# Kernel optimization log

Measured on AMD Instinct MI355X. Metric: run time of the kernel, lower is better.

## Reference

```python
import jax, jax.numpy as jnp
import numpy as np

C = 64
K = 3  # kernel_size
B, H, W = 8, 128, 128


def conv2d(x, w, b, pad, groups=1):
    y = jax.lax.conv_general_dilated(
        x, w, window_strides=(1, 1), padding=[(pad, pad), (pad, pad)],
        feature_group_count=groups, dimension_numbers=('NCHW', 'OIHW', 'NCHW'))
    return y + b[None, :, None, None]


def setup_inputs() -> dict:
    key = jax.random.key(0)
    ks = jax.random.split(key, 11)
    s3 = 1.0 / np.sqrt(C * 9)  # kaiming-ish scale for 3x3 convs
    inp = {
        'x':  jax.random.normal(ks[0], (B, C, H, W), jnp.float32),
        'w0': jax.random.normal(ks[1], (C, C, 3, 3), jnp.float32) * s3,
        'b0': jax.random.normal(ks[2], (C,), jnp.float32) * 0.01,
        'w1': jax.random.normal(ks[3], (C, 1, 3, 3), jnp.float32) * (1.0 / 3.0),  # depthwise
        'b1': jax.random.normal(ks[4], (C,), jnp.float32) * 0.01,
        'w2': jax.random.normal(ks[5], (1, 1, K), jnp.float32) * (1.0 / np.sqrt(K)),  # conv1d over channel axis
        'b2': jax.random.normal(ks[6], (1,), jnp.float32) * 0.01,
        'w3': jax.random.normal(ks[7], (C * K * K, C, 1, 1), jnp.float32) * (1.0 / np.sqrt(C)),  # 1x1 -> dynamic filters
        'b3': jax.random.normal(ks[8], (C * K * K,), jnp.float32) * 0.01,
        'wf': jax.random.normal(ks[9], (C, C, 3, 3), jnp.float32) * s3,
        'bf': jax.random.normal(ks[10], (C,), jnp.float32) * 0.01,
    }
    return inp


def reference(x, w0, b0, w1, b1, w2, b2, w3, b3, wf, bf):
    b, c, h, w = x.shape
    pre = x
    # conv0: dense 3x3
    x0 = conv2d(x, w0, b0, pad=1)
    # conv1: depthwise 3x3
    x1 = conv2d(x0, w1, b1, pad=1, groups=c)
    # ECA-style channel attention: global avg pool -> conv1d over channel dim
    m = jnp.mean(x0, axis=(2, 3))  # [b, c]
    x2 = jax.lax.conv_general_dilated(
        m[:, None, :], w2, window_strides=(1,), padding=[(K // 2, K // 2)],
        dimension_numbers=('NCH', 'OIH', 'NCH')) + b2[None, :, None]  # [b, 1, c]
    out = x1 + x2[:, 0, :, None, None]  # broadcast [b,c,1,1] over h,w
    # conv3: 1x1 producing per-pixel dynamic filters [b, c*9, h, w]
    fil = jnp.einsum('oc,bchw->bohw', w3[:, :, 0, 0], out) + b3[None, :, None, None]
    filter_x = fil.reshape(b, c, K * K, h, w)
    # unfold(x0): 3x3 patches, channel-major then row-major kernel positions
    xp = jnp.pad(x0, ((0, 0), (0, 0), (1, 1), (1, 1)))
    unfold_x = jnp.stack(
        [xp[:, :, i:i + h, j:j + w] for i in range(3) for j in range(3)], axis=2)  # [b,c,9,h,w]
    out = jnp.sum(unfold_x * filter_x, axis=2)  # per-pixel dynamic conv
    out = jnp.where(out >= 0, out, 0.2 * out)  # LeakyReLU(0.2)
    out = conv2d(out, wf, bf, pad=1) + pre
    return out
```

## Files before the change

### kernel.cpp

```cpp
#include <hip/hip_runtime.h>

#define BB 8
#define C 64
#define HH 128
#define WW 128
#define HW (HH*WW)

#define TS 72
#define NPX 324

typedef __attribute__((ext_vector_type(8))) short short8;
typedef __attribute__((ext_vector_type(4))) unsigned short us4;
typedef __attribute__((ext_vector_type(4))) float f32x4;

__device__ inline unsigned short f2bf(float f) {
    union { float f; unsigned u; } v; v.f = f;
    unsigned r = v.u + 0x7fff + ((v.u >> 16) & 1);
    return (unsigned short)(r >> 16);
}
__device__ inline float bf2f(unsigned short h) {
    union { unsigned u; float f; } v; v.u = ((unsigned)h) << 16;
    return v.f;
}

__global__ __launch_bounds__(256) void prep_kernel(
    const float* __restrict__ w0, const float* __restrict__ wf,
    const float* __restrict__ w3, const float* __restrict__ b3,
    unsigned short* __restrict__ wb0, unsigned short* __restrict__ wbf,
    unsigned short* __restrict__ wb3, float* __restrict__ b3r,
    float* __restrict__ m)
{
    const int t = blockIdx.x * 256 + threadIdx.x;
    for (int i = t; i < C*C*9; i += 128*256) {
        int p = i % 9; int rest = i / 9; int ci = rest % C; int oc = rest / C;
        wb0[(p*C + oc)*C + ci] = f2bf(w0[i]);
        wbf[(p*C + oc)*C + ci] = f2bf(wf[i]);
    }
    for (int i = t; i < 9*C*C; i += 128*256) {
        int j = i >> 12, oc = (i >> 6) & 63, k = i & 63;
        wb3[i] = f2bf(w3[(oc*9 + j)*C + k]);
    }
    for (int i = t; i < 9*C; i += 128*256) {
        int j = i >> 6, oc = i & 63;
        b3r[i] = b3[oc*9 + j];
    }
    for (int i = t; i < BB*C; i += 128*256) m[i] = 0.f;
}

template<bool FIRST>
__global__ __launch_bounds__(256) void conv_mfma_kernel(
    const void* __restrict__ in,
    const unsigned short* __restrict__ wb,
    const float* __restrict__ bias,
    const float* __restrict__ res,
    void* __restrict__ outp,
    float* __restrict__ m)
{
    __shared__ __align__(16) unsigned short tile[NPX*TS];
    __shared__ __align__(16) float sred[4][4][16];
    const int b  = blockIdx.z;
    const int h0 = blockIdx.y * 16;
    const int w0 = blockIdx.x * 16;
    const int t  = threadIdx.x;

    {
        const int pxi = t & 31, g = t >> 5;
        for (int px = pxi; px < NPX; px += 32) {
            int th = px / 18, tw = px - th*18;
            int gh = h0 + th - 1, gw = w0 + tw - 1;
            short8 v = {0,0,0,0,0,0,0,0};
            if ((unsigned)gh < HH && (unsigned)gw < WW) {
                if (FIRST) {
                    const float* sp = (const float*)in
                        + ((size_t)(b*C + g*8)*HW + gh*WW + gw);
#pragma unroll
                    for (int k = 0; k < 8; ++k) v[k] = (short)f2bf(sp[k*HW]);
                } else {
                    v = *(const short8*)((const unsigned short*)in
                        + ((size_t)(b*HW) + gh*WW + gw)*C + g*8);
                }
            }
            *(short8*)&tile[px*TS + g*8] = v;
        }
    }
    __syncthreads();

    const int wid = t >> 6, ln = t & 63;
    const int l15 = ln & 15, q = ln >> 4;

    f32x4 acc[4][4];
#pragma unroll
    for (int mg = 0; mg < 4; ++mg)
#pragma unroll
        for (int nt = 0; nt < 4; ++nt) acc[mg][nt] = (f32x4){0.f,0.f,0.f,0.f};

#pragma unroll
    for (int p = 0; p < 9; ++p) {
        const int dh = p / 3, dw = p % 3;
#pragma unroll
        for (int ks = 0; ks < 2; ++ks) {
            short8 bfrag[4];
#pragma unroll
            for (int nt = 0; nt < 4; ++nt)
                bfrag[nt] = *(const short8*)&wb[((size_t)(p*C) + nt*16 + l15)*C + ks*32 + q*8];
            short8 afrag[4];
#pragma unroll
            for (int mg = 0; mg < 4; ++mg) {
                const int r = wid*4 + mg;
                afrag[mg] = *(const short8*)&tile[((r+dh)*18 + l15 + dw)*TS + ks*32 + q*8];
            }
#pragma unroll
            for (int mg = 0; mg < 4; ++mg)
#pragma unroll
                for (int nt = 0; nt < 4; ++nt) {
                    if (FIRST)
                        acc[mg][nt] = __builtin_amdgcn_mfma_f32_16x16x32_bf16(
                            afrag[mg], bfrag[nt], acc[mg][nt], 0, 0, 0);
                    else
                        acc[mg][nt] = __builtin_amdgcn_mfma_f32_16x16x32_bf16(
                            bfrag[nt], afrag[mg], acc[mg][nt], 0, 0, 0);
                }
        }
    }

    if (FIRST) {
        unsigned short* x0o = (unsigned short*)outp;
#pragma unroll
        for (int nt = 0; nt < 4; ++nt) {
            const int oc = nt*16 + l15;
            const float bv = bias[oc];
            float s = 0.f;
#pragma unroll
            for (int mg = 0; mg < 4; ++mg) {
                const int hh = h0 + wid*4 + mg;
#pragma unroll
                for (int reg = 0; reg < 4; ++reg) {
                    const int wwp = w0 + q*4 + reg;
                    const unsigned short sv = f2bf(acc[mg][nt][reg] + bv);
                    x0o[((size_t)(b*HW) + hh*WW + wwp)*C + oc] = sv;
                    s += bf2f(sv);
                }
            }
            s += __shfl_xor(s, 16);
            s += __shfl_xor(s, 32);
            if (q == 0) sred[wid][nt][l15] = s;
        }
        __syncthreads();
        if (t < 64) {
            float s = sred[0][t >> 4][t & 15] + sred[1][t >> 4][t & 15]
                    + sred[2][t >> 4][t & 15] + sred[3][t >> 4][t & 15];
            atomicAdd(&m[b*C + t], s * (1.f/(float)HW));
        }
    } else {
        float* outg = (float*)outp;
#pragma unroll
        for (int mg = 0; mg < 4; ++mg) {
            const int hh = h0 + wid*4 + mg;
#pragma unroll
            for (int nt = 0; nt < 4; ++nt) {
                const f32x4 bv4 = *(const f32x4*)&bias[nt*16 + q*4];
#pragma unroll
                for (int reg = 0; reg < 4; ++reg) {
                    const int oc = nt*16 + q*4 + reg;
                    const size_t base = (size_t)(b*C + oc)*HW + hh*WW + w0 + l15;
                    outg[base] = acc[mg][nt][reg] + bv4[reg] + res[base];
                }
            }
        }
    }
}

__global__ __launch_bounds__(256) void fused_kernel(
    const unsigned short* __restrict__ x0,
    const float* __restrict__ w1, const float* __restrict__ b1,
    const float* __restrict__ w2, const float* __restrict__ b2,
    const unsigned short* __restrict__ wb3,
    const float* __restrict__ b3r,
    const float* __restrict__ m,
    unsigned short* __restrict__ y)
{
    __shared__ __align__(16) unsigned short tile[NPX*TS];
    __shared__ __align__(16) unsigned short alds[256*64];
    __shared__ __align__(16) float att[64];
    const int b  = blockIdx.z;
    const int h0 = blockIdx.y * 16;
    const int w0 = blockIdx.x * 16;
    const int t  = threadIdx.x;

    if (t < 64) {
        const float mc = m[b*C + t];
        const float mp = (t > 0)  ? m[b*C + t - 1] : 0.f;
        const float mn = (t < 63) ? m[b*C + t + 1] : 0.f;
        att[t] = b1[t] + fmaf(w2[0], mp, fmaf(w2[1], mc, fmaf(w2[2], mn, b2[0])));
    }
    {
        const int pxi = t & 31, g = t >> 5;
        for (int px = pxi; px < NPX; px += 32) {
            int th = px / 18, tw = px - th*18;
            int gh = h0 + th - 1, gw = w0 + tw - 1;
            short8 v = {0,0,0,0,0,0,0,0};
            if ((unsigned)gh < HH && (unsigned)gw < WW)
                v = *(const short8*)&x0[((size_t)(b*HW) + gh*WW + gw)*C + g*8];
            *(short8*)&tile[px*TS + g*8] = v;
        }
    }
    __syncthreads();

    const int r = t >> 4, cc = t & 15;
    const unsigned short* tbase = tile + (r*18 + cc)*TS;

    float outv[64];
#pragma unroll
    for (int g = 0; g < 8; ++g) {
        float dw8[8];
#pragma unroll
        for (int k = 0; k < 8; ++k) dw8[k] = 0.f;
#pragma unroll
        for (int j = 0; j < 9; ++j) {
            short8 v = *(const short8*)&tbase[((j/3)*18 + (j%3))*TS + g*8];
#pragma unroll
            for (int k = 0; k < 8; ++k)
                dw8[k] = fmaf(w1[(g*8+k)*9 + j], bf2f((unsigned short)v[k]), dw8[k]);
        }
#pragma unroll
        for (int k = 0; k < 8; ++k) {
            const int c = g*8 + k;
            outv[c] = dw8[k] + att[c];
        }
    }

    {
        const int sw = t & 7;
#pragma unroll
        for (int g = 0; g < 8; ++g) {
            short8 v;
#pragma unroll
            for (int k = 0; k < 8; ++k) v[k] = (short)f2bf(outv[g*8 + k]);
            *(short8*)&alds[t*64 + ((g ^ sw) * 8)] = v;
        }
    }
    __syncthreads();

    const int wid = t >> 6, ln = t & 63;
    const int l15 = ln & 15, q = ln >> 4;

    short8 afrag[4][2];
#pragma unroll
    for (int mg = 0; mg < 4; ++mg) {
        const int px = (wid*4 + mg)*16 + l15;
        const int sw = px & 7;
#pragma unroll
        for (int ks = 0; ks < 2; ++ks)
            afrag[mg][ks] = *(const short8*)&alds[px*64 + (((ks*4 + q) ^ sw) * 8)];
    }

    f32x4 y_acc[4][4];
#pragma unroll
    for (int mg = 0; mg < 4; ++mg)
#pragma unroll
        for (int nt = 0; nt < 4; ++nt) y_acc[mg][nt] = (f32x4){0.f,0.f,0.f,0.f};

#pragma unroll 1
    for (int j = 0; j < 9; ++j) {
        const int dh = j / 3, dw = j - dh*3;
#pragma unroll
        for (int ntoc = 0; ntoc < 4; ++ntoc) {
            const short8 bf0 = *(const short8*)&wb3[((size_t)(j*64 + ntoc*16 + l15))*64 + q*8];
            const short8 bf1 = *(const short8*)&wb3[((size_t)(j*64 + ntoc*16 + l15))*64 + 32 + q*8];
            const f32x4 b3v4 = *(const f32x4*)&b3r[j*64 + ntoc*16 + q*4];
#pragma unroll
            for (int mg = 0; mg < 4; ++mg) {
                f32x4 a = b3v4;
                a = __builtin_amdgcn_mfma_f32_16x16x32_bf16(bf0, afrag[mg][0], a, 0, 0, 0);
                a = __builtin_amdgcn_mfma_f32_16x16x32_bf16(bf1, afrag[mg][1], a, 0, 0, 0);
                const int rr = wid*4 + mg;
                const us4 pv = *(const us4*)
                    &tile[((rr+dh)*18 + l15 + dw)*TS + ntoc*16 + q*4];
#pragma unroll
                for (int reg = 0; reg < 4; ++reg)
                    y_acc[mg][ntoc][reg] = fmaf(a[reg], bf2f(pv[reg]), y_acc[mg][ntoc][reg]);
            }
        }
    }

    __syncthreads();
    unsigned short* ybuf = alds;
#pragma unroll
    for (int mg = 0; mg < 4; ++mg) {
        const int rr = wid*4 + mg;
        const int px = rr*16 + l15;
        const int swy = (px & 7) << 1;
#pragma unroll
        for (int ntoc = 0; ntoc < 4; ++ntoc) {
            us4 ov;
#pragma unroll
            for (int reg = 0; reg < 4; ++reg) {
                float v = y_acc[mg][ntoc][reg];
                v = (v >= 0.f) ? v : 0.2f * v;
                ov[reg] = f2bf(v);
            }
            const int slot = (ntoc*4 + q) ^ swy;
            *(us4*)&ybuf[px*64 + slot*4] = ov;
        }
    }
    __syncthreads();
    for (int id = t; id < 2048; id += 256) {
        int px = id >> 3, g = id & 7;
        const int swy = (px & 7) << 1;
        short8 v = *(const short8*)&ybuf[px*64 + ((2*g) ^ swy)*4];
        int rr = px >> 4, cw = px & 15;
        *(short8*)&y[((size_t)(b*HW) + (h0+rr)*WW + (w0+cw))*C + g*8] = v;
    }
}

extern "C" void kernel_launch(void* const* d_in, const int* in_sizes, int n_in,
                              void* d_out, int out_size, void* d_ws, size_t ws_size,
                              hipStream_t stream) {
    const float* x  = (const float*)d_in[0];
    const float* w0 = (const float*)d_in[1];
    const float* b0 = (const float*)d_in[2];
    const float* w1 = (const float*)d_in[3];
    const float* b1 = (const float*)d_in[4];
    const float* w2 = (const float*)d_in[5];
    const float* b2 = (const float*)d_in[6];
    const float* w3 = (const float*)d_in[7];
    const float* b3 = (const float*)d_in[8];
    const float* wf = (const float*)d_in[9];
    const float* bf = (const float*)d_in[10];
    float* out = (float*)d_out;

    unsigned short* x0  = (unsigned short*)d_ws;
    unsigned short* y   = x0 + (size_t)BB*HW*C;
    float*          m   = (float*)(y + (size_t)BB*HW*C);
    unsigned short* wb0 = (unsigned short*)(m + BB*C);
    unsigned short* wbf = wb0 + 9*C*C;
    unsigned short* wb3 = wbf + 9*C*C;
    float*          b3r = (float*)(wb3 + 9*C*C);

    prep_kernel<<<128, 256, 0, stream>>>(w0, wf, w3, b3, wb0, wbf, wb3, b3r, m);
    conv_mfma_kernel<true><<<dim3(8,8,8), 256, 0, stream>>>(x, wb0, b0, nullptr, x0, m);
    fused_kernel<<<dim3(8,8,8), 256, 0, stream>>>(x0, w1, b1, w2, b2, wb3, b3r, m, y);
    conv_mfma_kernel<false><<<dim3(8,8,8), 256, 0, stream>>>(y, wbf, bf, x, out, nullptr);
}
```

Measured before the change: 214.0 us.

## Halve spatial tile height and split output channels across wave pairs

Shrinks each block's tile from 16x16 to 8x16 pixels and doubles the grid. Waves now split work 2x2 by row group and output-channel half, and the depthwise stage splits channels across two thread halves. This cuts per-block LDS and accumulator registers, and the grid grows to 1024 blocks, which should raise occupancy and CU coverage on a 256-CU part. In exchange the halo is a larger share of each tile, adding redundant loads, and each wave reloads A fragments for fewer output channels.

```diff
diff --git a/kernel.cpp b/kernel.cpp
--- a/kernel.cpp
+++ b/kernel.cpp
@@ -7,7 +7,7 @@
 #define HW (HH*WW)
 
 #define TS 72
-#define NPX 324
+#define NPX 180
 
 typedef __attribute__((ext_vector_type(8))) short short8;
 typedef __attribute__((ext_vector_type(4))) unsigned short us4;
@@ -57,9 +57,9 @@
     float* __restrict__ m)
 {
     __shared__ __align__(16) unsigned short tile[NPX*TS];
-    __shared__ __align__(16) float sred[4][4][16];
+    __shared__ __align__(16) float sred[2][2][2][16];
     const int b  = blockIdx.z;
-    const int h0 = blockIdx.y * 16;
+    const int h0 = blockIdx.y * 8;
     const int w0 = blockIdx.x * 16;
     const int t  = threadIdx.x;
 
@@ -87,32 +87,33 @@
 
     const int wid = t >> 6, ln = t & 63;
     const int l15 = ln & 15, q = ln >> 4;
-
-    f32x4 acc[4][4];
+    const int ng = wid & 1, wr = wid >> 1;
+
+    f32x4 acc[4][2];
 #pragma unroll
     for (int mg = 0; mg < 4; ++mg)
 #pragma unroll
-        for (int nt = 0; nt < 4; ++nt) acc[mg][nt] = (f32x4){0.f,0.f,0.f,0.f};
+        for (int nt = 0; nt < 2; ++nt) acc[mg][nt] = (f32x4){0.f,0.f,0.f,0.f};
 
 #pragma unroll
     for (int p = 0; p < 9; ++p) {
         const int dh = p / 3, dw = p % 3;
 #pragma unroll
         for (int ks = 0; ks < 2; ++ks) {
-            short8 bfrag[4];
-#pragma unroll
-            for (int nt = 0; nt < 4; ++nt)
-                bfrag[nt] = *(const short8*)&wb[((size_t)(p*C) + nt*16 + l15)*C + ks*32 + q*8];
+            short8 bfrag[2];
+#pragma unroll
+            for (int nt = 0; nt < 2; ++nt)
+                bfrag[nt] = *(const short8*)&wb[((size_t)(p*C) + ng*32 + nt*16 + l15)*C + ks*32 + q*8];
             short8 afrag[4];
 #pragma unroll
             for (int mg = 0; mg < 4; ++mg) {
-                const int r = wid*4 + mg;
+                const int r = wr*4 + mg;
                 afrag[mg] = *(const short8*)&tile[((r+dh)*18 + l15 + dw)*TS + ks*32 + q*8];
             }
 #pragma unroll
             for (int mg = 0; mg < 4; ++mg)
 #pragma unroll
-                for (int nt = 0; nt < 4; ++nt) {
+                for (int nt = 0; nt < 2; ++nt) {
                     if (FIRST)
                         acc[mg][nt] = __builtin_amdgcn_mfma_f32_16x16x32_bf16(
                             afrag[mg], bfrag[nt], acc[mg][nt], 0, 0, 0);
@@ -126,13 +127,13 @@
     if (FIRST) {
         unsigned short* x0o = (unsigned short*)outp;
 #pragma unroll
-        for (int nt = 0; nt < 4; ++nt) {
-            const int oc = nt*16 + l15;
+        for (int nt = 0; nt < 2; ++nt) {
+            const int oc = ng*32 + nt*16 + l15;
             const float bv = bias[oc];
             float s = 0.f;
 #pragma unroll
             for (int mg = 0; mg < 4; ++mg) {
-                const int hh = h0 + wid*4 + mg;
+                const int hh = h0 + wr*4 + mg;
 #pragma unroll
                 for (int reg = 0; reg < 4; ++reg) {
                     const int wwp = w0 + q*4 + reg;
@@ -143,25 +144,25 @@
             }
             s += __shfl_xor(s, 16);
             s += __shfl_xor(s, 32);
-            if (q == 0) sred[wid][nt][l15] = s;
+            if (q == 0) sred[ng][nt][wr][l15] = s;
         }
         __syncthreads();
         if (t < 64) {
-            float s = sred[0][t >> 4][t & 15] + sred[1][t >> 4][t & 15]
-                    + sred[2][t >> 4][t & 15] + sred[3][t >> 4][t & 15];
+            const int g2 = t >> 5, nt2 = (t >> 4) & 1, l2 = t & 15;
+            float s = sred[g2][nt2][0][l2] + sred[g2][nt2][1][l2];
             atomicAdd(&m[b*C + t], s * (1.f/(float)HW));
         }
     } else {
         float* outg = (float*)outp;
 #pragma unroll
         for (int mg = 0; mg < 4; ++mg) {
-            const int hh = h0 + wid*4 + mg;
-#pragma unroll
-            for (int nt = 0; nt < 4; ++nt) {
-                const f32x4 bv4 = *(const f32x4*)&bias[nt*16 + q*4];
+            const int hh = h0 + wr*4 + mg;
+#pragma unroll
+            for (int nt = 0; nt < 2; ++nt) {
+                const f32x4 bv4 = *(const f32x4*)&bias[ng*32 + nt*16 + q*4];
 #pragma unroll
                 for (int reg = 0; reg < 4; ++reg) {
-                    const int oc = nt*16 + q*4 + reg;
+                    const int oc = ng*32 + nt*16 + q*4 + reg;
                     const size_t base = (size_t)(b*C + oc)*HW + hh*WW + w0 + l15;
                     outg[base] = acc[mg][nt][reg] + bv4[reg] + res[base];
                 }
@@ -180,10 +181,10 @@
     unsigned short* __restrict__ y)
 {
     __shared__ __align__(16) unsigned short tile[NPX*TS];
-    __shared__ __align__(16) unsigned short alds[256*64];
+    __shared__ __align__(16) unsigned short alds[128*64];
     __shared__ __align__(16) float att[64];
     const int b  = blockIdx.z;
-    const int h0 = blockIdx.y * 16;
+    const int h0 = blockIdx.y * 8;
     const int w0 = blockIdx.x * 16;
     const int t  = threadIdx.x;
 
@@ -206,79 +207,74 @@
     }
     __syncthreads();
 
-    const int r = t >> 4, cc = t & 15;
-    const unsigned short* tbase = tile + (r*18 + cc)*TS;
-
-    float outv[64];
-#pragma unroll
-    for (int g = 0; g < 8; ++g) {
-        float dw8[8];
-#pragma unroll
-        for (int k = 0; k < 8; ++k) dw8[k] = 0.f;
-#pragma unroll
-        for (int j = 0; j < 9; ++j) {
-            short8 v = *(const short8*)&tbase[((j/3)*18 + (j%3))*TS + g*8];
+    {
+        const int px1 = t & 127, chalf = t >> 7;
+        const int r1 = px1 >> 4, c1 = px1 & 15;
+        const unsigned short* tbase = tile + (r1*18 + c1)*TS + chalf*32;
+        const int sw1 = px1 & 7;
+#pragma unroll
+        for (int g = 0; g < 4; ++g) {
+            float dw8[8];
+#pragma unroll
+            for (int k = 0; k < 8; ++k) dw8[k] = 0.f;
+#pragma unroll
+            for (int j = 0; j < 9; ++j) {
+                short8 v = *(const short8*)&tbase[((j/3)*18 + (j%3))*TS + g*8];
+#pragma unroll
+                for (int k = 0; k < 8; ++k)
+                    dw8[k] = fmaf(w1[(chalf*32 + g*8 + k)*9 + j],
+                                  bf2f((unsigned short)v[k]), dw8[k]);
+            }
+            short8 ov;
 #pragma unroll
             for (int k = 0; k < 8; ++k)
-                dw8[k] = fmaf(w1[(g*8+k)*9 + j], bf2f((unsigned short)v[k]), dw8[k]);
-        }
-#pragma unroll
-        for (int k = 0; k < 8; ++k) {
-            const int c = g*8 + k;
-            outv[c] = dw8[k] + att[c];
-        }
-    }
-
-    {
-        const int sw = t & 7;
-#pragma unroll
-        for (int g = 0; g < 8; ++g) {
-            short8 v;
-#pragma unroll
-            for (int k = 0; k < 8; ++k) v[k] = (short)f2bf(outv[g*8 + k]);
-            *(short8*)&alds[t*64 + ((g ^ sw) * 8)] = v;
+                ov[k] = (short)f2bf(dw8[k] + att[chalf*32 + g*8 + k]);
+            const int kg = chalf*4 + g;
+            *(short8*)&alds[px1*64 + ((kg ^ sw1) * 8)] = ov;
         }
     }
     __syncthreads();
 
     const int wid = t >> 6, ln = t & 63;
     const int l15 = ln & 15, q = ln >> 4;
+    const int ng = wid & 1, wr = wid >> 1;
 
     short8 afrag[4][2];
 #pragma unroll
     for (int mg = 0; mg < 4; ++mg) {
-        const int px = (wid*4 + mg)*16 + l15;
+        const int px = (wr*4 + mg)*16 + l15;
         const int sw = px & 7;
 #pragma unroll
         for (int ks = 0; ks < 2; ++ks)
             afrag[mg][ks] = *(const short8*)&alds[px*64 + (((ks*4 + q) ^ sw) * 8)];
     }
 
-    f32x4 y_acc[4][4];
+    f32x4 y_acc[4][2];
 #pragma unroll
     for (int mg = 0; mg < 4; ++mg)
 #pragma unroll
-        for (int nt = 0; nt < 4; ++nt) y_acc[mg][nt] = (f32x4){0.f,0.f,0.f,0.f};
+        for (int nt = 0; nt < 2; ++nt) y_acc[mg][nt] = (f32x4){0.f,0.f,0.f,0.f};
 
 #pragma unroll 1
     for (int j = 0; j < 9; ++j) {
         const int dh = j / 3, dw = j - dh*3;
 #pragma unroll
-        for (int ntoc = 0; ntoc < 4; ++ntoc) {
-            const short8 bf0 = *(const short8*)&wb3[((size_t)(j*64 + ntoc*16 + l15))*64 + q*8];
-            const short8 bf1 = *(const short8*)&wb3[((size_t)(j*64 + ntoc*16 + l15))*64 + 32 + q*8];
-            const f32x4 b3v4 = *(const f32x4*)&b3r[j*64 + ntoc*16 + q*4];
+        for (int nt = 0; nt < 2; ++nt) {
+            const int octile = ng*2 + nt;
+            const short8 bf0 = *(const short8*)&wb3[((size_t)(j*64 + octile*16 + l15))*64 + q*8];
+            const short8 bf1 = *(const short8*)&wb3[((size_t)(j*64 + octile*16 + l15))*64 + 32 + q*8];
+            const f32x4 b3v4 = *(const f32x4*)&b3r[j*64 + octile*16 + q*4];
 #pragma unroll
             for (int mg = 0; mg < 4; ++mg) {
                 f32x4 a = b3v4;
                 a = __builtin_amdgcn_mfma_f32_16x16x32_bf16(bf0, afrag[mg][0], a, 0, 0, 0);
                 a = __builtin_amdgcn_mfma_f32_16x16x32_bf16(bf1, afrag[mg][1], a, 0, 0, 0);
-                const int rr = wid*4 + mg;
+                const int rr = wr*4 + mg;
                 const us4 pv = *(const us4*)
-                    &tile[((rr+dh)*18 + l15 + dw)*TS + ntoc*16 + q*4];
+                    &tile[((rr+dh)*18 + l15 + dw)*TS + octile*16 + q*4];
 #pragma unroll
                 for (int reg = 0; reg < 4; ++reg)
-                    y_acc[mg][ntoc][reg] = fmaf(a[reg], bf2f(pv[reg]), y_acc[mg][ntoc][reg]);
+                    y_acc[mg][nt][reg] = fmaf(a[reg], bf2f(pv[reg]), y_acc[mg][nt][reg]);
             }
         }
     }
@@ -287,24 +283,24 @@
     unsigned short* ybuf = alds;
 #pragma unroll
     for (int mg = 0; mg < 4; ++mg) {
-        const int rr = wid*4 + mg;
+        const int rr = wr*4 + mg;
         const int px = rr*16 + l15;
         const int swy = (px & 7) << 1;
 #pragma unroll
-        for (int ntoc = 0; ntoc < 4; ++ntoc) {
+        for (int nt = 0; nt < 2; ++nt) {
             us4 ov;
 #pragma unroll
             for (int reg = 0; reg < 4; ++reg) {
-                float v = y_acc[mg][ntoc][reg];
+                float v = y_acc[mg][nt][reg];
                 v = (v >= 0.f) ? v : 0.2f * v;
                 ov[reg] = f2bf(v);
             }
-            const int slot = (ntoc*4 + q) ^ swy;
+            const int slot = ((ng*2 + nt)*4 + q) ^ swy;
             *(us4*)&ybuf[px*64 + slot*4] = ov;
         }
     }
     __syncthreads();
-    for (int id = t; id < 2048; id += 256) {
+    for (int id = t; id < 1024; id += 256) {
         int px = id >> 3, g = id & 7;
         const int swy = (px & 7) << 1;
         short8 v = *(const short8*)&ybuf[px*64 + ((2*g) ^ swy)*4];
@@ -338,7 +334,7 @@
     float*          b3r = (float*)(wb3 + 9*C*C);
 
     prep_kernel<<<128, 256, 0, stream>>>(w0, wf, w3, b3, wb0, wbf, wb3, b3r, m);
-    conv_mfma_kernel<true><<<dim3(8,8,8), 256, 0, stream>>>(x, wb0, b0, nullptr, x0, m);
-    fused_kernel<<<dim3(8,8,8), 256, 0, stream>>>(x0, w1, b1, w2, b2, wb3, b3r, m, y);
-    conv_mfma_kernel<false><<<dim3(8,8,8), 256, 0, stream>>>(y, wbf, bf, x, out, nullptr);
-}
+    conv_mfma_kernel<true><<<dim3(8,16,8), 256, 0, stream>>>(x, wb0, b0, nullptr, x0, m);
+    fused_kernel<<<dim3(8,16,8), 256, 0, stream>>>(x0, w1, b1, w2, b2, wb3, b3r, m, y);
+    conv_mfma_kernel<false><<<dim3(8,16,8), 256, 0, stream>>>(y, wbf, bf, x, out, nullptr);
+}
```

After: 209.3 us. -2.2%, faster.
